# Kernel tuning notes

Measured on AMD Instinct MI355X. Metric: run time of the kernel, lower is better.

The kernel has to match this reference:

```python
import jax, jax.numpy as jnp
import numpy as np

UNITS = 64
CHANNEL = 64
L1 = 32
L2 = 32
BATCH = 64


def setup_inputs() -> dict:
    key = jax.random.key(0)
    k1, k2, k3, k4, k5 = jax.random.split(key, 5)
    input_dim = CHANNEL + 3 * UNITS
    inputs = jax.random.normal(k1, (BATCH, CHANNEL, L1, L2), dtype=jnp.float32)
    W = jax.random.normal(k2, (input_dim, UNITS * 7), dtype=jnp.float32) * (1.0 / np.sqrt(input_dim))
    U_rec = jax.random.normal(k3, (UNITS * 3, UNITS), dtype=jnp.float32) * (1.0 / np.sqrt(UNITS * 3))
    bias = jnp.zeros((UNITS * 8,), dtype=jnp.float32)
    W_ij = jax.random.normal(k4, (CHANNEL, UNITS), dtype=jnp.float32) * (1.0 / np.sqrt(CHANNEL))
    return {"inputs": inputs, "W": W, "U_rec": U_rec, "bias": bias, "W_ij": W_ij}


def reference(inputs, W, U_rec, bias, W_ij):
    B, C, l1, l2 = inputs.shape
    u = W_ij.shape[1]
    wr, br = W[:, : 3 * u], bias[: 3 * u]
    wz, bz = W[:, 3 * u : 7 * u], bias[3 * u : 7 * u]
    b_ij = bias[7 * u :]

    # [L1*L2, B, C] scan order: row-major over (i, j), direction 'lt'
    x = jnp.transpose(inputs, (2, 3, 0, 1)).reshape(l1 * l2, B, C)
    states0 = jnp.zeros((l1 + 1, l2 + 1, B, u), dtype=inputs.dtype)  # zero boundary

    def step(carry, xs):
        states, _ = carry
        s_ij, t = xs
        i = t // l2
        j = t % l2
        h_diag = states[i, j]        # [B, u]
        h_top = states[i, j + 1]
        h_left = states[i + 1, j]
        # q = [h_top, h_left, h_diag, s_ij] : [B, 3u + C]
        q = jnp.concatenate([h_top, h_left, h_diag, s_ij], axis=1)
        r = jax.nn.sigmoid(q @ wr + br)                     # [B, 3u]
        z = q @ wz + bz                                     # [B, 4u]
        zg = jax.nn.softmax(z.reshape(B, 4, u), axis=1)     # softmax across 4 gates per unit
        zi, zl, zt, zd = zg[:, 0], zg[:, 1], zg[:, 2], zg[:, 3]
        h_hat = jnp.tanh(
            s_ij @ W_ij + b_ij
            + (r * jnp.concatenate([h_left, h_top, h_diag], axis=1)) @ U_rec
        )
        h_ij = zl * h_left + zt * h_top + zd * h_diag + zi * h_hat
        states = states.at[i + 1, j + 1].set(h_ij)
        return (states, h_ij), None

    tsteps = jnp.arange(l1 * l2)
    (_, h_last), _ = jax.lax.scan(
        step, (states0, jnp.zeros((B, u), dtype=inputs.dtype)), (x, tsteps)
    )
    return h_last
```

## Files before the change

kernel.cpp:

```cpp
#include <hip/hip_runtime.h>
#include <cstdint>
#include <cstddef>


#define LDIM   32
#define BATCH  64
#define UNITS  64
#define CHAN   64
#define NBT    4
#define BT     16
#define TPB    512

typedef _Float16 f16;
typedef _Float16 f16x8 __attribute__((ext_vector_type(8)));
typedef float    f32x4 __attribute__((ext_vector_type(4)));

__global__ __launch_bounds__(TPB, 2) void spatial_gru_kernel(
    const float* __restrict__ x,
    const float* __restrict__ W,
    const float* __restrict__ Urec,
    const float* __restrict__ bias,
    const float* __restrict__ Wij,
    float* __restrict__ out,
    int* __restrict__ flags,
    float* __restrict__ states)
{
    const int bid = blockIdx.x;
    const int row = bid >> 2;
    const int bt  = bid & 3;
    const int b0  = bt * BT;
    const int t   = (int)threadIdx.x;
    const int u   = t & 63;
    const int g   = t >> 6;
    const int l15 = t & 15;
    const int lq  = (t & 63) >> 4;

    __shared__ __attribute__((aligned(16))) f16 qf[BT][264];
    __shared__ __attribute__((aligned(16))) f16 rf[BT][264];
    __shared__ float qs32[BT][204];
    __shared__ float Gsz [BT][260];
    __shared__ float pacc[4][BT][68];

    f16x8 wreg[4][8];
    float bias1[4] = {0.f, 0.f, 0.f, 0.f};
    if (g < 7) {
        const int nb = g * 64 + l15;
#pragma unroll
        for (int T = 0; T < 4; ++T) {
            bias1[T] = bias[nb + 16 * T];
#pragma unroll
            for (int s = 0; s < 8; ++s) {
                f16x8 v;
#pragma unroll
                for (int jj = 0; jj < 8; ++jj) {
                    int kk = s * 32 + lq * 8 + jj;
                    v[jj] = (f16)W[(size_t)kk * 448 + nb + 16 * T];
                }
                wreg[T][s] = v;
            }
        }
    }
    f16x8 wreg2[4][2];
    {
        const int kb = (g & 3) * 64;
#pragma unroll
        for (int T = 0; T < 4; ++T) {
            const int nn = T * 16 + l15;
#pragma unroll
            for (int s = 0; s < 2; ++s) {
                f16x8 v;
#pragma unroll
                for (int jj = 0; jj < 8; ++jj) {
                    int kk = kb + s * 32 + lq * 8 + jj;
                    float wv = (kk < 192) ? Urec[kk * 64 + nn] : Wij[(kk - 192) * 64 + nn];
                    v[jj] = (f16)wv;
                }
                wreg2[T][s] = v;
            }
        }
    }
    const float bij = bias[448 + u];

    for (int idx = t; idx < 192 * BT; idx += TPB) {
        int b = idx & 15, k = idx >> 4;
        qs32[b][k] = 0.f;
        qf[b][k] = (f16)0.f;
    }

    const size_t xb0 = (size_t)(b0 + g) * 65536 + (size_t)u * 1024 + (size_t)row * 32;
    const size_t xb1 = xb0 + (size_t)8 * 65536;
    {
        float x0 = x[xb0], x1 = x[xb1];
        qf[g][192 + u]     = (f16)x0;  rf[g][192 + u]     = (f16)x0;
        qf[g + 8][192 + u] = (f16)x1;  rf[g + 8][192 + u] = (f16)x1;
    }
    __syncthreads();

    for (int j = 0; j < LDIM; ++j) {
        float nx0 = 0.f, nx1 = 0.f;
        if (j < LDIM - 1) { nx0 = x[xb0 + j + 1]; nx1 = x[xb1 + j + 1]; }

        f32x4 acc[4];
        if (g < 7) {
#pragma unroll
            for (int T = 0; T < 4; ++T)
                acc[T] = (f32x4){bias1[T], bias1[T], bias1[T], bias1[T]};
#pragma unroll
            for (int s = 2; s < 8; ++s) {
                f16x8 a = *(const f16x8*)&qf[l15][s * 32 + lq * 8];
#pragma unroll
                for (int T = 0; T < 4; ++T)
                    acc[T] = __builtin_amdgcn_mfma_f32_16x16x32_f16(a, wreg[T][s], acc[T], 0, 0, 0);
            }
        } else {
            f32x4 a2[4];
#pragma unroll
            for (int T = 0; T < 4; ++T) a2[T] = (f32x4){0.f, 0.f, 0.f, 0.f};
#pragma unroll
            for (int s = 0; s < 2; ++s) {
                f16x8 a = *(const f16x8*)&rf[l15][192 + s * 32 + lq * 8];
#pragma unroll
                for (int T = 0; T < 4; ++T)
                    a2[T] = __builtin_amdgcn_mfma_f32_16x16x32_f16(a, wreg2[T][s], a2[T], 0, 0, 0);
            }
#pragma unroll
            for (int T = 0; T < 4; ++T)
#pragma unroll
                for (int r = 0; r < 4; ++r)
                    pacc[3][lq * 4 + r][T * 16 + l15] = a2[T][r];
        }

        float ht0 = 0.f, ht1 = 0.f;
        if (row > 0) {
            const int* fl = flags + (((row - 1) * LDIM + j) * NBT + bt) * 8 + g;
            while (__hip_atomic_load(fl, __ATOMIC_RELAXED, __HIP_MEMORY_SCOPE_AGENT) != 1) {
                __builtin_amdgcn_s_sleep(1);
            }
            asm volatile("" ::: "memory");
            const float* sp = states + (((size_t)(row - 1) * LDIM + j) * BATCH + b0) * UNITS;
            ht0 = __hip_atomic_load(sp + (size_t)g * 64 + u,
                                    __ATOMIC_RELAXED, __HIP_MEMORY_SCOPE_AGENT);
            ht1 = __hip_atomic_load(sp + (size_t)(g + 8) * 64 + u,
                                    __ATOMIC_RELAXED, __HIP_MEMORY_SCOPE_AGENT);
        }
        qs32[g][u]     = ht0;  qf[g][u]     = (f16)ht0;
        qs32[g + 8][u] = ht1;  qf[g + 8][u] = (f16)ht1;
        __syncthreads();

        if (g < 7) {
#pragma unroll
            for (int s = 0; s < 2; ++s) {
                f16x8 a = *(const f16x8*)&qf[l15][s * 32 + lq * 8];
#pragma unroll
                for (int T = 0; T < 4; ++T)
                    acc[T] = __builtin_amdgcn_mfma_f32_16x16x32_f16(a, wreg[T][s], acc[T], 0, 0, 0);
            }
            if (g < 3) {
                const int colbase = (g == 0) ? 64 : (g == 1) ? 0 : 128;
#pragma unroll
                for (int T = 0; T < 4; ++T)
#pragma unroll
                    for (int r = 0; r < 4; ++r) {
                        float rr = 1.f / (1.f + __expf(-acc[T][r]));
                        int b = lq * 4 + r;
                        float hv = qs32[b][colbase + T * 16 + l15];
                        rf[b][g * 64 + T * 16 + l15] = (f16)(rr * hv);
                    }
            } else {
                const int zb = (g - 3) * 64;
#pragma unroll
                for (int T = 0; T < 4; ++T)
#pragma unroll
                    for (int r = 0; r < 4; ++r)
                        Gsz[lq * 4 + r][zb + T * 16 + l15] = acc[T][r];
            }
        }
        __syncthreads();

        if (g >= 4 && g < 7) {
            const int w  = g - 4;
            const int kb = w * 64;
            f32x4 a2[4];
#pragma unroll
            for (int T = 0; T < 4; ++T) a2[T] = (f32x4){0.f, 0.f, 0.f, 0.f};
#pragma unroll
            for (int s = 0; s < 2; ++s) {
                f16x8 a = *(const f16x8*)&rf[l15][kb + s * 32 + lq * 8];
#pragma unroll
                for (int T = 0; T < 4; ++T)
                    a2[T] = __builtin_amdgcn_mfma_f32_16x16x32_f16(a, wreg2[T][s], a2[T], 0, 0, 0);
            }
#pragma unroll
            for (int T = 0; T < 4; ++T)
#pragma unroll
                for (int r = 0; r < 4; ++r)
                    pacc[w][lq * 4 + r][T * 16 + l15] = a2[T][r];
        }
        __syncthreads();

        float hvv[2], hTv[2];
#pragma unroll
        for (int i = 0; i < 2; ++i) {
            int b = g + 8 * i;
            float hhv = bij + pacc[0][b][u] + pacc[1][b][u] + pacc[2][b][u] + pacc[3][b][u];
            float e2 = __expf(2.f * hhv);
            float th = 1.f - 2.f / (e2 + 1.f);
            float zi = Gsz[b][u],       zl = Gsz[b][64 + u];
            float zt = Gsz[b][128 + u], zd = Gsz[b][192 + u];
            float mx = fmaxf(fmaxf(zi, zl), fmaxf(zt, zd));
            float ei = __expf(zi - mx), el = __expf(zl - mx);
            float et = __expf(zt - mx), ed = __expf(zd - mx);
            float inv = 1.f / (ei + el + et + ed);
            float hT = qs32[b][u], hL = qs32[b][64 + u], hD = qs32[b][128 + u];
            float hv = (el * hL + et * hT + ed * hD + ei * th) * inv;
            hvv[i] = hv; hTv[i] = hT;
            __hip_atomic_store(
                states + (((size_t)row * LDIM + j) * BATCH + b0 + b) * UNITS + u,
                hv, __ATOMIC_RELAXED, __HIP_MEMORY_SCOPE_AGENT);
        }
        if (row == LDIM - 1 && j == LDIM - 1) {
            out[(size_t)(b0 + g) * UNITS + u]     = hvv[0];
            out[(size_t)(b0 + g + 8) * UNITS + u] = hvv[1];
        }
#pragma unroll
        for (int i = 0; i < 2; ++i) {
            int b = g + 8 * i;
            qs32[b][128 + u] = hTv[i];
            qs32[b][64 + u]  = hvv[i];
            f16 htf = qf[b][u];
            qf[b][128 + u] = htf;
            qf[b][64 + u]  = (f16)hvv[i];
        }
        qf[g][192 + u]     = (f16)nx0;  rf[g][192 + u]     = (f16)nx0;
        qf[g + 8][192 + u] = (f16)nx1;  rf[g + 8][192 + u] = (f16)nx1;

        asm volatile("s_waitcnt vmcnt(0)" ::: "memory");
        if (u == 0) {
            __hip_atomic_store(flags + ((row * LDIM + j) * NBT + bt) * 8 + g, 1,
                               __ATOMIC_RELAXED, __HIP_MEMORY_SCOPE_AGENT);
        }
        __syncthreads();
    }
}

extern "C" void kernel_launch(void* const* d_in, const int* in_sizes, int n_in,
                              void* d_out, int out_size, void* d_ws, size_t ws_size,
                              hipStream_t stream) {
    const float* x    = (const float*)d_in[0];
    const float* W    = (const float*)d_in[1];
    const float* Urec = (const float*)d_in[2];
    const float* bias = (const float*)d_in[3];
    const float* Wij  = (const float*)d_in[4];
    float* out = (float*)d_out;

    int*   flags  = (int*)d_ws;
    float* states = (float*)((char*)d_ws + 131072);

    spatial_gru_kernel<<<LDIM * NBT, TPB, 0, stream>>>(
        x, W, Urec, bias, Wij, out, flags, states);
}
```

Baseline: 309.1 us.

## Pack fp16 hidden-state pairs with embedded ready bits to replace separate flags

Each thread now publishes its two fp16 hidden values as one 32-bit word, with the low mantissa bit forced to 1 as a ready marker. The consumer spins on that word directly. This removes the separate flag store, the vmcnt(0) drain and one block barrier per step, cutting the producer-to-consumer handoff to a single global round trip. The loop is also reordered to wait for the upper row before running all eight MFMA k-slices. The input projection now reads qf directly, so the rf copy of x is dropped. In exchange, the upper-row state is passed in fp16 with a perturbed LSB. The x and bias MFMAs also no longer overlap the wait on the upper row.

Measured after the change: 263.7 us. -14.7%, faster.

```diff
diff --git a/kernel.cpp b/kernel.cpp
--- a/kernel.cpp
+++ b/kernel.cpp
@@ -22,8 +22,7 @@
     const float* __restrict__ bias,
     const float* __restrict__ Wij,
     float* __restrict__ out,
-    int* __restrict__ flags,
-    float* __restrict__ states)
+    uint32_t* __restrict__ hbuf)
 {
     const int bid = blockIdx.x;
     const int row = bid >> 2;
@@ -36,7 +35,7 @@
     const int lq  = (t & 63) >> 4;
 
     __shared__ __attribute__((aligned(16))) f16 qf[BT][264];
-    __shared__ __attribute__((aligned(16))) f16 rf[BT][264];
+    __shared__ __attribute__((aligned(16))) f16 rf[BT][200];
     __shared__ float qs32[BT][204];
     __shared__ float Gsz [BT][260];
     __shared__ float pacc[4][BT][68];
@@ -91,65 +90,42 @@
     const size_t xb1 = xb0 + (size_t)8 * 65536;
     {
         float x0 = x[xb0], x1 = x[xb1];
-        qf[g][192 + u]     = (f16)x0;  rf[g][192 + u]     = (f16)x0;
-        qf[g + 8][192 + u] = (f16)x1;  rf[g + 8][192 + u] = (f16)x1;
+        qf[g][192 + u]     = (f16)x0;
+        qf[g + 8][192 + u] = (f16)x1;
     }
     __syncthreads();
 
     for (int j = 0; j < LDIM; ++j) {
+        float ht0 = 0.f, ht1 = 0.f;
+        f16 hf0 = (f16)0.f, hf1 = (f16)0.f;
+        if (row > 0) {
+            const uint32_t* sp =
+                hbuf + ((((size_t)(row - 1) * LDIM + j) * NBT + bt) << 9) + (g << 6) + u;
+            uint32_t w = __hip_atomic_load(sp, __ATOMIC_RELAXED, __HIP_MEMORY_SCOPE_AGENT);
+            while ((w & 0x00010001u) != 0x00010001u) {
+                __builtin_amdgcn_s_sleep(1);
+                w = __hip_atomic_load(sp, __ATOMIC_RELAXED, __HIP_MEMORY_SCOPE_AGENT);
+            }
+            uint16_t lo = (uint16_t)(w & 0xFFFFu), hi = (uint16_t)(w >> 16);
+            hf0 = __builtin_bit_cast(f16, lo);
+            hf1 = __builtin_bit_cast(f16, hi);
+            ht0 = (float)hf0;
+            ht1 = (float)hf1;
+        }
+        qs32[g][u]     = ht0;  qf[g][u]     = hf0;
+        qs32[g + 8][u] = ht1;  qf[g + 8][u] = hf1;
+        __syncthreads();
+
         float nx0 = 0.f, nx1 = 0.f;
         if (j < LDIM - 1) { nx0 = x[xb0 + j + 1]; nx1 = x[xb1 + j + 1]; }
 
-        f32x4 acc[4];
         if (g < 7) {
+            f32x4 acc[4];
 #pragma unroll
             for (int T = 0; T < 4; ++T)
                 acc[T] = (f32x4){bias1[T], bias1[T], bias1[T], bias1[T]};
 #pragma unroll
-            for (int s = 2; s < 8; ++s) {
-                f16x8 a = *(const f16x8*)&qf[l15][s * 32 + lq * 8];
-#pragma unroll
-                for (int T = 0; T < 4; ++T)
-                    acc[T] = __builtin_amdgcn_mfma_f32_16x16x32_f16(a, wreg[T][s], acc[T], 0, 0, 0);
-            }
-        } else {
-            f32x4 a2[4];
-#pragma unroll
-            for (int T = 0; T < 4; ++T) a2[T] = (f32x4){0.f, 0.f, 0.f, 0.f};
-#pragma unroll
-            for (int s = 0; s < 2; ++s) {
-                f16x8 a = *(const f16x8*)&rf[l15][192 + s * 32 + lq * 8];
-#pragma unroll
-                for (int T = 0; T < 4; ++T)
-                    a2[T] = __builtin_amdgcn_mfma_f32_16x16x32_f16(a, wreg2[T][s], a2[T], 0, 0, 0);
-            }
-#pragma unroll
-            for (int T = 0; T < 4; ++T)
-#pragma unroll
-                for (int r = 0; r < 4; ++r)
-                    pacc[3][lq * 4 + r][T * 16 + l15] = a2[T][r];
-        }
-
-        float ht0 = 0.f, ht1 = 0.f;
-        if (row > 0) {
-            const int* fl = flags + (((row - 1) * LDIM + j) * NBT + bt) * 8 + g;
-            while (__hip_atomic_load(fl, __ATOMIC_RELAXED, __HIP_MEMORY_SCOPE_AGENT) != 1) {
-                __builtin_amdgcn_s_sleep(1);
-            }
-            asm volatile("" ::: "memory");
-            const float* sp = states + (((size_t)(row - 1) * LDIM + j) * BATCH + b0) * UNITS;
-            ht0 = __hip_atomic_load(sp + (size_t)g * 64 + u,
-                                    __ATOMIC_RELAXED, __HIP_MEMORY_SCOPE_AGENT);
-            ht1 = __hip_atomic_load(sp + (size_t)(g + 8) * 64 + u,
-                                    __ATOMIC_RELAXED, __HIP_MEMORY_SCOPE_AGENT);
-        }
-        qs32[g][u]     = ht0;  qf[g][u]     = (f16)ht0;
-        qs32[g + 8][u] = ht1;  qf[g + 8][u] = (f16)ht1;
-        __syncthreads();
-
-        if (g < 7) {
-#pragma unroll
-            for (int s = 0; s < 2; ++s) {
+            for (int s = 0; s < 8; ++s) {
                 f16x8 a = *(const f16x8*)&qf[l15][s * 32 + lq * 8];
 #pragma unroll
                 for (int T = 0; T < 4; ++T)
@@ -174,6 +150,22 @@
                     for (int r = 0; r < 4; ++r)
                         Gsz[lq * 4 + r][zb + T * 16 + l15] = acc[T][r];
             }
+        } else {
+            f32x4 a2[4];
+#pragma unroll
+            for (int T = 0; T < 4; ++T) a2[T] = (f32x4){0.f, 0.f, 0.f, 0.f};
+#pragma unroll
+            for (int s = 0; s < 2; ++s) {
+                f16x8 a = *(const f16x8*)&qf[l15][192 + s * 32 + lq * 8];
+#pragma unroll
+                for (int T = 0; T < 4; ++T)
+                    a2[T] = __builtin_amdgcn_mfma_f32_16x16x32_f16(a, wreg2[T][s], a2[T], 0, 0, 0);
+            }
+#pragma unroll
+            for (int T = 0; T < 4; ++T)
+#pragma unroll
+                for (int r = 0; r < 4; ++r)
+                    pacc[3][lq * 4 + r][T * 16 + l15] = a2[T][r];
         }
         __syncthreads();
 
@@ -214,9 +206,14 @@
             float hT = qs32[b][u], hL = qs32[b][64 + u], hD = qs32[b][128 + u];
             float hv = (el * hL + et * hT + ed * hD + ei * th) * inv;
             hvv[i] = hv; hTv[i] = hT;
+        }
+        {
+            uint16_t lo = (uint16_t)(__builtin_bit_cast(uint16_t, (f16)hvv[0]) | 1u);
+            uint16_t hi = (uint16_t)(__builtin_bit_cast(uint16_t, (f16)hvv[1]) | 1u);
+            uint32_t pw = ((uint32_t)hi << 16) | lo;
             __hip_atomic_store(
-                states + (((size_t)row * LDIM + j) * BATCH + b0 + b) * UNITS + u,
-                hv, __ATOMIC_RELAXED, __HIP_MEMORY_SCOPE_AGENT);
+                hbuf + ((((size_t)row * LDIM + j) * NBT + bt) << 9) + (g << 6) + u,
+                pw, __ATOMIC_RELAXED, __HIP_MEMORY_SCOPE_AGENT);
         }
         if (row == LDIM - 1 && j == LDIM - 1) {
             out[(size_t)(b0 + g) * UNITS + u]     = hvv[0];
@@ -231,15 +228,8 @@
             qf[b][128 + u] = htf;
             qf[b][64 + u]  = (f16)hvv[i];
         }
-        qf[g][192 + u]     = (f16)nx0;  rf[g][192 + u]     = (f16)nx0;
-        qf[g + 8][192 + u] = (f16)nx1;  rf[g + 8][192 + u] = (f16)nx1;
-
-        asm volatile("s_waitcnt vmcnt(0)" ::: "memory");
-        if (u == 0) {
-            __hip_atomic_store(flags + ((row * LDIM + j) * NBT + bt) * 8 + g, 1,
-                               __ATOMIC_RELAXED, __HIP_MEMORY_SCOPE_AGENT);
-        }
-        __syncthreads();
+        qf[g][192 + u]     = (f16)nx0;
+        qf[g + 8][192 + u] = (f16)nx1;
     }
 }
 
@@ -253,9 +243,8 @@
     const float* Wij  = (const float*)d_in[4];
     float* out = (float*)d_out;
 
-    int*   flags  = (int*)d_ws;
-    float* states = (float*)((char*)d_ws + 131072);
+    uint32_t* hbuf = (uint32_t*)d_ws;
 
     spatial_gru_kernel<<<LDIM * NBT, TPB, 0, stream>>>(
-        x, W, Urec, bias, Wij, out, flags, states);
+        x, W, Urec, bias, Wij, out, hbuf);
 }
```
